# Performance work log

Hardware: AMD Instinct MI355X
Metric: run time of the kernel (lower is better)

## Reference

```python
import jax, jax.numpy as jnp
import numpy as np

NUM_SLOTS = 8
SLOT_DIM = 3
WRITE_RATE = 0.1


def _amu(x, memory, Wk, bk, Ww, bw, Wg, bg, Wo, bo):
    """Associative Memory Unit.
    x: [B, T, Din], memory: [B, N, D] -> (outputs [B, T, Dout], memory [B, N, D]).
    Per step: softmax key-addressing read, gated erase/add write at WRITE_RATE,
    output = Linear(concat(x_t, read)).
    """
    xt = jnp.swapaxes(x, 0, 1)  # [T, B, Din]

    def step(mem, x_t):
        k = x_t @ Wk + bk                                   # [B, D]
        scores = jnp.einsum('bnd,bd->bn', mem, k)           # [B, N]
        w = jax.nn.softmax(scores, axis=-1)                 # addressing weights
        read = jnp.einsum('bn,bnd->bd', w, mem)             # [B, D]
        v = x_t @ Ww + bw                                   # write vector [B, D]
        e = jax.nn.sigmoid(x_t @ Wg + bg)                   # erase gate [B, D]
        we = w[:, :, None] * e[:, None, :]                  # [B, N, D]
        mem = mem * (1.0 - WRITE_RATE * we) + WRITE_RATE * w[:, :, None] * v[:, None, :]
        out = jnp.concatenate([x_t, read], axis=-1) @ Wo + bo
        return mem, out

    mem, outs = jax.lax.scan(step, memory, xt)
    return jnp.swapaxes(outs, 0, 1), mem


def setup_inputs() -> dict:
    key = jax.random.key(0)
    ks = jax.random.split(key, 12)
    B, T, D_in, D_hid, D_out = 64, 512, 128, 512, 128
    s = 0.05
    return {
        'inp': jax.random.normal(ks[0], (B, T, D_in), jnp.float32),
        'W1k': jax.random.normal(ks[1], (D_in, SLOT_DIM), jnp.float32) * s,
        'b1k': jnp.zeros((SLOT_DIM,), jnp.float32),
        'W1w': jax.random.normal(ks[2], (D_in, SLOT_DIM), jnp.float32) * s,
        'b1w': jnp.zeros((SLOT_DIM,), jnp.float32),
        'W1g': jax.random.normal(ks[3], (D_in, SLOT_DIM), jnp.float32) * s,
        'b1g': jnp.zeros((SLOT_DIM,), jnp.float32),
        'W1o': jax.random.normal(ks[4], (D_in + SLOT_DIM, D_hid), jnp.float32) * s,
        'b1o': jnp.zeros((D_hid,), jnp.float32),
        'W2k': jax.random.normal(ks[5], (D_hid, SLOT_DIM), jnp.float32) * s,
        'b2k': jnp.zeros((SLOT_DIM,), jnp.float32),
        'W2w': jax.random.normal(ks[6], (D_hid, SLOT_DIM), jnp.float32) * s,
        'b2w': jnp.zeros((SLOT_DIM,), jnp.float32),
        'W2g': jax.random.normal(ks[7], (D_hid, SLOT_DIM), jnp.float32) * s,
        'b2g': jnp.zeros((SLOT_DIM,), jnp.float32),
        'W2o': jax.random.normal(ks[8], (D_hid + SLOT_DIM, D_out), jnp.float32) * s,
        'b2o': jnp.zeros((D_out,), jnp.float32),
    }


def reference(inp, W1k, b1k, W1w, b1w, W1g, b1g, W1o, b1o,
              W2k, b2k, W2w, b2w, W2g, b2g, W2o, b2o):
    B = inp.shape[0]
    mem0 = jnp.zeros((B, NUM_SLOTS, SLOT_DIM), inp.dtype)
    o1, mem = _amu(inp, mem0, W1k, b1k, W1w, b1w, W1g, b1g, W1o, b1o)
    o1 = jax.nn.sigmoid(o1)  # self.layers = Sequential(Sigmoid())
    o2, mem = _amu(o1, mem, W2k, b2k, W2w, b2w, W2g, b2g, W2o, b2o)
    out = jax.nn.sigmoid(o2[:, -1, :])  # last timestep, then sigmoid
    return out
```

## Files before the change

kernel.cpp:

```cpp
#include <hip/hip_runtime.h>
#include <hip/hip_bf16.h>

#define B_ 64
#define T_ 512
#define LOG2E 1.4426950408889634f
#define PHASE_STEPS 16
#define NPHASE (T_/PHASE_STEPS)

typedef __attribute__((ext_vector_type(8))) short short8;
typedef __attribute__((ext_vector_type(4))) float f32x4;

__device__ __forceinline__ float fast_exp2(float x){ return __builtin_amdgcn_exp2f(x); }
__device__ __forceinline__ float fast_rcp(float x){ return __builtin_amdgcn_rcpf(x); }
__device__ __forceinline__ float sigmoidf_(float x){ return fast_rcp(1.0f + fast_exp2(-x*LOG2E)); }
__device__ __forceinline__ unsigned short f2bf(float f){
  union{float f; unsigned u;} v; v.f = f;
  unsigned r = v.u + 0x7fffu + ((v.u>>16)&1u);
  return (unsigned short)(r>>16);
}
__device__ __forceinline__ float bf2f(unsigned short u){
  union{unsigned u; float f;} v; v.u = ((unsigned)u)<<16; return v.f;
}

template<int CTRL>
__device__ __forceinline__ float dpp_xadd(float x){
  int y = __builtin_amdgcn_update_dpp(0, __float_as_int(x), CTRL, 0xf, 0xf, true);
  return x + __int_as_float(y);
}
__device__ __forceinline__ float dpp_sum8(float x){
  x = dpp_xadd<0xB1>(x);
  x = dpp_xadd<0x4E>(x);
  x = dpp_xadd<0x141>(x);
  return x;
}

__device__ __forceinline__ void lds_barrier(){
  asm volatile("s_waitcnt lgkmcnt(0)" ::: "memory");
  __builtin_amdgcn_s_barrier();
  asm volatile("" ::: "memory");
}

__global__ __launch_bounds__(256) void k_proj1(const float* __restrict__ X,
    const float* __restrict__ Wk, const float* __restrict__ bk,
    const float* __restrict__ Ww, const float* __restrict__ bw,
    const float* __restrict__ Wg, const float* __restrict__ bg,
    float* __restrict__ P1,
    const float* __restrict__ W1o,
    const float* __restrict__ W2k, const float* __restrict__ W2w, const float* __restrict__ W2g,
    unsigned short* __restrict__ W1oTb, unsigned short* __restrict__ W2cTb)
{
  __shared__ __align__(16) float A[64*132];
  __shared__ __align__(16) float WcT[9*132];
  __shared__ float bb[9];
  int tid = threadIdx.x;
  if (blockIdx.x >= 512){
    int idx = ((int)blockIdx.x - 512)*256 + tid;
    if (idx < 65536){
      int n = idx >> 7, k = idx & 127;
      W1oTb[idx] = f2bf(W1o[k*512 + n]);
    }
    if (idx < 8192){
      int j = idx >> 9, c = idx & 511;
      float v = 0.f;
      if (j < 3) v = W2k[c*3 + j];
      else if (j < 6) v = W2w[c*3 + j - 3];
      else if (j < 9) v = W2g[c*3 + j - 6];
      W2cTb[idx] = f2bf(v);
    }
    return;
  }
  long r0 = (long)blockIdx.x * 64;
  const float4* X4 = (const float4*)(X + r0*128);
  #pragma unroll
  for (int it=0; it<8; ++it){
    int f4 = tid + it*256;
    float4 v = X4[f4];
    int f = f4*4; int row = f>>7; int k = f&127;
    *(float4*)&A[row*132+k] = v;
  }
  #pragma unroll
  for (int it=0; it<5; ++it){
    int w0 = tid + it*256;
    if (w0 < 1152){
      int k = w0/9, j = w0%9;
      float val;
      if (j<3) val = Wk[k*3+j]; else if (j<6) val = Ww[k*3+j-3]; else val = Wg[k*3+j-6];
      WcT[j*132+k] = val;
    }
  }
  if (tid < 9){
    float v; if (tid<3) v = bk[tid]; else if (tid<6) v = bw[tid-3]; else v = bg[tid-6];
    bb[tid] = v;
  }
  __syncthreads();
  for (int o = tid; o < 576; o += 256){
    int row = o/9, j = o%9;
    const f32x4* Ar = (const f32x4*)(A + row*132);
    const f32x4* Wr = (const f32x4*)(WcT + j*132);
    f32x4 acc4 = {0.f,0.f,0.f,0.f};
    #pragma unroll
    for (int k4=0;k4<32;++k4){
      f32x4 a = Ar[k4], wv = Wr[k4];
      acc4[0]=fmaf(a[0],wv[0],acc4[0]);
      acc4[1]=fmaf(a[1],wv[1],acc4[1]);
      acc4[2]=fmaf(a[2],wv[2],acc4[2]);
      acc4[3]=fmaf(a[3],wv[3],acc4[3]);
    }
    float acc = bb[j] + (acc4[0]+acc4[1]) + (acc4[2]+acc4[3]);
    if (j<3) acc *= LOG2E;
    else if (j<6) acc *= 0.1f;
    else acc = 0.1f * sigmoidf_(acc);
    long r = r0 + row;
    int b = (int)(r >> 9); int t = (int)(r & 511);
    int bh = b >> 5, bl = b & 31;
    P1[(((long)bh*512 + t)*32 + bl)*12 + j] = acc;
  }
}

template<int STORE_SM>
__device__ __forceinline__ void scan_slim(const float* __restrict__ P,
                                          float* __restrict__ Out, int bh)
{
  __shared__ __align__(16) float buf[2][PHASE_STEPS*32*12];
  int tid = threadIdx.x;
  int wv = tid >> 6, lane = tid & 63;
  const float* Pb = P + (long)bh*512*384;
  if (wv == 8){
    #pragma unroll 1
    for (int p = 0; p < NPHASE; ++p){
      const float4* s4 = (const float4*)Pb + (long)p*1536;
      float4* d4 = (float4*)buf[p&1];
      #pragma unroll
      for (int c=0;c<2;++c){
        float4 tmp[12];
        #pragma unroll
        for (int i=0;i<12;++i) tmp[i] = s4[lane + (c*12+i)*64];
        #pragma unroll
        for (int i=0;i<12;++i) d4[lane + (c*12+i)*64] = tmp[i];
      }
      lds_barrier();
    }
    return;
  }
  if (lane >= 32) return;
  int g = lane >> 3, slot = lane & 7;
  int bl = wv*4 + g;
  int batch = bh*32 + bl;
  float* So = Out + ((long)batch*8 + slot)*4;
  float m0=0.f, m1=0.f, m2=0.f;
  f32x4 pfa[4], pfb[4]; float pfc[4];
  lds_barrier();
  #pragma unroll 1
  for (int p = 0; p < NPHASE; ++p){
    const float* bp = buf[p&1] + bl*12;
    const f32x4* bp4 = (const f32x4*)bp;
    #pragma unroll
    for (int u=0;u<3;++u){
      pfa[u]=bp4[u*96]; pfb[u]=bp4[u*96+1]; pfc[u]=bp[u*384+8];
    }
    #pragma unroll
    for (int s=0;s<PHASE_STEPS;++s){
      f32x4 A0=pfa[s&3], A1=pfb[s&3]; float e2=pfc[s&3];
      if (s+3 < PHASE_STEPS){
        int i3=(s+3)&3;
        pfa[i3]=bp4[(s+3)*96]; pfb[i3]=bp4[(s+3)*96+1]; pfc[i3]=bp[(s+3)*384+8];
      }
      float sc = fmaf(m2, A0[2], fmaf(m1, A0[1], m0*A0[0]));
      float pe = fast_exp2(sc);
      float S = dpp_sum8(pe);
      float rinv = fast_rcp(S);
      float w = pe * rinv;
      if (STORE_SM){
        f32x4 sv; sv[0]=pe; sv[1]=m0; sv[2]=m1; sv[3]=m2;
        *(f32x4*)(So + (long)(p*PHASE_STEPS+s)*2048) = sv;
      } else if (p == NPHASE-1 && s == PHASE_STEPS-1){
        float r0 = dpp_sum8(pe*m0);
        float r1 = dpp_sum8(pe*m1);
        float r2 = dpp_sum8(pe*m2);
        float rsel = (slot==0) ? r0 : ((slot==1) ? r1 : r2);
        rsel *= rinv;
        if (slot < 3) Out[slot*64 + batch] = rsel;
      }
      float v0=A0[3], v1=A1[0], v2=A1[1], e0=A1[2], e1=A1[3];
      m0 = fmaf(w, fmaf(-e0, m0, v0), m0);
      m1 = fmaf(w, fmaf(-e1, m1, v1), m1);
      m2 = fmaf(w, fmaf(-e2, m2, v2), m2);
    }
    if (p < NPHASE-1) lds_barrier();
  }
}

__global__ __launch_bounds__(576) void k_scan1(const float* __restrict__ P1,
                                               float* __restrict__ SM)
{
  scan_slim<1>(P1, SM, (int)blockIdx.x);
}

__global__ __launch_bounds__(256) void k_fused(const float* __restrict__ X,
    const float* __restrict__ W1o, const float* __restrict__ b1o,
    const float* __restrict__ SM,
    const unsigned short* __restrict__ W1oTb, const unsigned short* __restrict__ W2cTb,
    const float* __restrict__ b2k, const float* __restrict__ b2w, const float* __restrict__ b2g,
    float* __restrict__ P2, float* __restrict__ O1last)
{
  __shared__ __align__(16) float rdS[192];
  __shared__ __align__(16) unsigned short o1b[64*520];
  __shared__ __align__(16) float pSum[4*16*16];
  int tid = threadIdx.x;
  int w = tid >> 6, lane = tid & 63;
  int n16 = lane & 15, g4 = lane >> 4;
  long r0 = (long)blockIdx.x * 64;
  int b = (int)(r0 >> 9); int t0 = (int)(r0 & 511);

  #pragma unroll
  for (int half=0; half<2; ++half){
    int i = (tid >> 3) + half*32;
    int slot = tid & 7;
    f32x4 v = *(const f32x4*)(SM + (((long)(t0+i)*64 + b)*8 + slot)*4);
    float S   = dpp_sum8(v[0]);
    float r0v = dpp_sum8(v[0]*v[1]);
    float r1v = dpp_sum8(v[0]*v[2]);
    float r2v = dpp_sum8(v[0]*v[3]);
    float rinv = fast_rcp(S);
    float rsel = (slot==0) ? r0v : ((slot==1) ? r1v : r2v);
    if (slot < 3) rdS[i*3+slot] = rsel*rinv;
  }

  short8 afr[4][4];
  #pragma unroll
  for (int rt=0; rt<4; ++rt){
    const float* Xrow = X + (r0 + rt*16 + n16)*128;
    #pragma unroll
    for (int q=0;q<4;++q){
      f32x4 x0 = *(const f32x4*)(Xrow + q*32 + g4*8);
      f32x4 x1 = *(const f32x4*)(Xrow + q*32 + g4*8 + 4);
      short8 a;
      a[0]=(short)f2bf(x0[0]); a[1]=(short)f2bf(x0[1]);
      a[2]=(short)f2bf(x0[2]); a[3]=(short)f2bf(x0[3]);
      a[4]=(short)f2bf(x1[0]); a[5]=(short)f2bf(x1[1]);
      a[6]=(short)f2bf(x1[2]); a[7]=(short)f2bf(x1[3]);
      afr[rt][q]=a;
    }
  }
  __syncthreads();

  #pragma unroll
  for (int tt=0; tt<8; ++tt){
    int gc = w*128 + tt*16 + n16;
    short8 bf[4];
    #pragma unroll
    for (int q=0;q<4;++q)
      bf[q] = *(const short8*)(W1oTb + gc*128 + q*32 + g4*8);
    float bias = b1o[gc];
    float wr0 = W1o[128*512+gc], wr1 = W1o[129*512+gc], wr2 = W1o[130*512+gc];
    #pragma unroll
    for (int rt=0; rt<4; ++rt){
      f32x4 acc = {0.f,0.f,0.f,0.f};
      #pragma unroll
      for (int q=0;q<4;++q)
        acc = __builtin_amdgcn_mfma_f32_16x16x32_bf16(afr[rt][q], bf[q], acc, 0,0,0);
      f32x4 ra = *(const f32x4*)(rdS + rt*48 + g4*12);
      f32x4 rb = *(const f32x4*)(rdS + rt*48 + g4*12 + 4);
      f32x4 rc = *(const f32x4*)(rdS + rt*48 + g4*12 + 8);
      float rd0[4] = { ra[0], ra[3], rb[2], rc[1] };
      float rd1[4] = { ra[1], rb[0], rb[3], rc[2] };
      float rd2[4] = { ra[2], rb[1], rc[0], rc[3] };
      #pragma unroll
      for (int reg=0; reg<4; ++reg){
        int rowloc = rt*16 + g4*4 + reg;
        float z = acc[reg] + bias + rd0[reg]*wr0 + rd1[reg]*wr1 + rd2[reg]*wr2;
        float o1 = sigmoidf_(z);
        o1b[rowloc*520 + gc] = f2bf(o1);
        if (t0 == 448 && rowloc == 63) O1last[b*512 + gc] = o1;
      }
    }
  }
  __syncthreads();

  #pragma unroll 1
  for (int rt2=0; rt2<4; ++rt2){
    f32x4 accP = {0.f,0.f,0.f,0.f};
    #pragma unroll
    for (int q2=0; q2<4; ++q2){
      int kk = w*128 + q2*32;
      short8 a2 = *(const short8*)(o1b + (rt2*16 + n16)*520 + kk + g4*8);
      short8 bb2 = *(const short8*)(W2cTb + n16*512 + kk + g4*8);
      accP = __builtin_amdgcn_mfma_f32_16x16x32_bf16(a2, bb2, accP, 0,0,0);
    }
    #pragma unroll
    for (int reg=0;reg<4;++reg){
      int rowloc = g4*4+reg;
      pSum[w*256 + rowloc*16 + n16] = accP[reg];
    }
    __syncthreads();
    if (tid < 144){
      int r = tid/9, j = tid%9;
      float s = pSum[r*16+j] + pSum[256+r*16+j] + pSum[512+r*16+j] + pSum[768+r*16+j];
      float outv;
      if (j<3){ s += b2k[j]; outv = s*LOG2E; }
      else if (j<6){ s += b2w[j-3]; outv = 0.1f*s; }
      else { s += b2g[j-6]; outv = 0.1f*sigmoidf_(s); }
      int t = t0 + rt2*16 + r;
      int bh = b >> 5, bl = b & 31;
      P2[(((long)bh*512 + t)*32 + bl)*12 + j] = outv;
    }
    __syncthreads();
  }
}

__global__ __launch_bounds__(576) void k_scan2_opart(const float* __restrict__ P2,
    float* __restrict__ R2F,
    const float* __restrict__ O1last, const float* __restrict__ W2o,
    const float* __restrict__ b2o, float* __restrict__ Opart)
{
  if (blockIdx.x < 2){
    scan_slim<0>(P2, R2F, (int)blockIdx.x);
    return;
  }
  __shared__ __align__(16) float s2[512];
  int b = blockIdx.x - 2; int tid = threadIdx.x;
  if (tid < 128)
    ((float4*)s2)[tid] = ((const float4*)(O1last + b*512))[tid];
  __syncthreads();
  if (tid < 128){
    float acc = b2o[tid];
    #pragma unroll 8
    for (int n=0;n<512;++n) acc = fmaf(s2[n], W2o[n*128+tid], acc);
    Opart[b*128+tid] = acc;
  }
}

__global__ __launch_bounds__(256) void k_final(const float* __restrict__ Opart,
    const float* __restrict__ R2F, const float* __restrict__ W2o,
    float* __restrict__ out)
{
  int idx = blockIdx.x*256 + threadIdx.x;
  if (idx < 8192){
    int b = idx >> 7; int o = idx & 127;
    float r0 = R2F[b], r1 = R2F[64+b], r2 = R2F[128+b];
    float v = Opart[idx]
            + r0*W2o[512*128+o] + r1*W2o[513*128+o] + r2*W2o[514*128+o];
    out[idx] = sigmoidf_(v);
  }
}

extern "C" void kernel_launch(void* const* d_in, const int* in_sizes, int n_in,
                              void* d_out, int out_size, void* d_ws, size_t ws_size,
                              hipStream_t stream)
{
  const float* X  = (const float*)d_in[0];
  const float* W1k= (const float*)d_in[1]; const float* b1k=(const float*)d_in[2];
  const float* W1w= (const float*)d_in[3]; const float* b1w=(const float*)d_in[4];
  const float* W1g= (const float*)d_in[5]; const float* b1g=(const float*)d_in[6];
  const float* W1o= (const float*)d_in[7]; const float* b1o=(const float*)d_in[8];
  const float* W2k= (const float*)d_in[9]; const float* b2k=(const float*)d_in[10];
  const float* W2w= (const float*)d_in[11]; const float* b2w=(const float*)d_in[12];
  const float* W2g= (const float*)d_in[13]; const float* b2g=(const float*)d_in[14];
  const float* W2o= (const float*)d_in[15]; const float* b2o=(const float*)d_in[16];

  float* ws = (float*)d_ws;
  float* P1     = ws;
  float* SM     = P1 + 393216;
  float* O1last = SM + 1048576;
  float* R2F    = O1last + 32768;
  float* Opart  = R2F + 192;
  unsigned short* W1oTb = (unsigned short*)(Opart + 8192);
  unsigned short* W2cTb = W1oTb + 65536;
  float* P2     = P1;
  float* out    = (float*)d_out;

  hipLaunchKernelGGL(k_proj1, dim3(768), dim3(256), 0, stream,
                     X, W1k,b1k, W1w,b1w, W1g,b1g, P1,
                     W1o, W2k, W2w, W2g, W1oTb, W2cTb);
  hipLaunchKernelGGL(k_scan1, dim3(2), dim3(576), 0, stream, P1, SM);
  hipLaunchKernelGGL(k_fused, dim3(512), dim3(256), 0, stream,
                     X, W1o, b1o, SM, W1oTb, W2cTb, b2k, b2w, b2g, P2, O1last);
  hipLaunchKernelGGL(k_scan2_opart, dim3(66), dim3(576), 0, stream,
                     P2, R2F, O1last, W2o, b2o, Opart);
  hipLaunchKernelGGL(k_final, dim3(32), dim3(256), 0, stream,
                     Opart, R2F, W2o, out);
}
```

Baseline: 226.0 us.

## Merge scans and fused projection into one flag-pipelined persistent kernel

Replaces the separate scan1, fused projection and scan2 launches with a single kernel. Two blocks run the first recurrent scan and publish per-chunk progress flags. Projection blocks spin on those flags before consuming softmax state, then bump counters that gate the second scan's loader warp. This lets the serial scans overlap with the bulk MFMA projection work and removes launch boundaries. The last-row output partial is also computed from LDS instead of a round trip through global memory. In exchange it relies on all producer blocks being co-resident, uses spin-waits, and writes P2 into the P1 buffer while scan1 may still be reading other timesteps of it.

```diff
diff --git a/kernel.cpp b/kernel.cpp
--- a/kernel.cpp
+++ b/kernel.cpp
@@ -6,6 +6,7 @@
 #define LOG2E 1.4426950408889634f
 #define PHASE_STEPS 16
 #define NPHASE (T_/PHASE_STEPS)
+#define AGENT_ __HIP_MEMORY_SCOPE_AGENT
 
 typedef __attribute__((ext_vector_type(8))) short short8;
 typedef __attribute__((ext_vector_type(4))) float f32x4;
@@ -40,6 +41,10 @@
   asm volatile("" ::: "memory");
 }
 
+__device__ __forceinline__ int aload(const int* p){
+  return __hip_atomic_load(p, __ATOMIC_ACQUIRE, AGENT_);
+}
+
 __global__ __launch_bounds__(256) void k_proj1(const float* __restrict__ X,
     const float* __restrict__ Wk, const float* __restrict__ bk,
     const float* __restrict__ Ww, const float* __restrict__ bw,
@@ -47,13 +52,15 @@
     float* __restrict__ P1,
     const float* __restrict__ W1o,
     const float* __restrict__ W2k, const float* __restrict__ W2w, const float* __restrict__ W2g,
-    unsigned short* __restrict__ W1oTb, unsigned short* __restrict__ W2cTb)
+    unsigned short* __restrict__ W1oTb, unsigned short* __restrict__ W2cTb,
+    int* __restrict__ flags)
 {
   __shared__ __align__(16) float A[64*132];
   __shared__ __align__(16) float WcT[9*132];
   __shared__ float bb[9];
   int tid = threadIdx.x;
   if (blockIdx.x >= 512){
+    if (blockIdx.x == 512 && tid < 18) flags[tid] = 0;
     int idx = ((int)blockIdx.x - 512)*256 + tid;
     if (idx < 65536){
       int n = idx >> 7, k = idx & 127;
@@ -117,17 +124,22 @@
   }
 }
 
-template<int STORE_SM>
-__device__ __forceinline__ void scan_slim(const float* __restrict__ P,
-                                          float* __restrict__ Out, int bh)
+template<int ROLE>
+__device__ __forceinline__ void scan_pipe(char* pool, const float* P,
+                                          float* __restrict__ Out, int bh,
+                                          int* flags)
 {
-  __shared__ __align__(16) float buf[2][PHASE_STEPS*32*12];
+  float (*buf)[PHASE_STEPS*32*12] = (float(*)[PHASE_STEPS*32*12])pool;
   int tid = threadIdx.x;
   int wv = tid >> 6, lane = tid & 63;
   const float* Pb = P + (long)bh*512*384;
   if (wv == 8){
     #pragma unroll 1
     for (int p = 0; p < NPHASE; ++p){
+      if (ROLE == 2 && (p&3)==0){
+        const int* f = flags + 2 + bh*8 + (p>>2);
+        while (aload(f) < 32) __builtin_amdgcn_s_sleep(8);
+      }
       const float4* s4 = (const float4*)Pb + (long)p*1536;
       float4* d4 = (float4*)buf[p&1];
       #pragma unroll
@@ -140,6 +152,7 @@
       }
       lds_barrier();
     }
+    if (ROLE == 1) lds_barrier();
     return;
   }
   if (lane >= 32) return;
@@ -170,7 +183,7 @@
       float S = dpp_sum8(pe);
       float rinv = fast_rcp(S);
       float w = pe * rinv;
-      if (STORE_SM){
+      if (ROLE == 1){
         f32x4 sv; sv[0]=pe; sv[1]=m0; sv[2]=m1; sv[3]=m2;
         *(f32x4*)(So + (long)(p*PHASE_STEPS+s)*2048) = sv;
       } else if (p == NPHASE-1 && s == PHASE_STEPS-1){
@@ -186,92 +199,110 @@
       m1 = fmaf(w, fmaf(-e1, m1, v1), m1);
       m2 = fmaf(w, fmaf(-e2, m2, v2), m2);
     }
+    if (ROLE == 1 && (p&3)==3)
+      asm volatile("s_waitcnt vmcnt(0)" ::: "memory");
     if (p < NPHASE-1) lds_barrier();
-  }
-}
-
-__global__ __launch_bounds__(576) void k_scan1(const float* __restrict__ P1,
-                                               float* __restrict__ SM)
-{
-  scan_slim<1>(P1, SM, (int)blockIdx.x);
-}
-
-__global__ __launch_bounds__(256) void k_fused(const float* __restrict__ X,
-    const float* __restrict__ W1o, const float* __restrict__ b1o,
-    const float* __restrict__ SM,
+    else if (ROLE == 1) lds_barrier();
+    if (ROLE == 1 && (p&3)==3 && tid==0)
+      __hip_atomic_store(&flags[bh], p+1, __ATOMIC_RELEASE, AGENT_);
+  }
+}
+
+__global__ __launch_bounds__(576) void k_pipe(
+    const float* P1, float* __restrict__ SM,
+    float* P2, float* __restrict__ R2F,
+    const float* __restrict__ X, const float* __restrict__ W1o, const float* __restrict__ b1o,
     const unsigned short* __restrict__ W1oTb, const unsigned short* __restrict__ W2cTb,
     const float* __restrict__ b2k, const float* __restrict__ b2w, const float* __restrict__ b2g,
-    float* __restrict__ P2, float* __restrict__ O1last)
+    const float* __restrict__ W2o, const float* __restrict__ b2o,
+    float* __restrict__ Opart, int* flags)
 {
-  __shared__ __align__(16) float rdS[192];
-  __shared__ __align__(16) unsigned short o1b[64*520];
-  __shared__ __align__(16) float pSum[4*16*16];
+  __shared__ __align__(16) char pool[73728];
+  int bid = blockIdx.x;
+  if (bid < 2){ scan_pipe<1>(pool, P1, SM, bid, flags); return; }
+  if (bid < 4){ scan_pipe<2>(pool, P2, R2F, bid-2, flags); return; }
+
+  float* rdS = (float*)pool;
+  unsigned short* o1b = (unsigned short*)(pool + 768);
+  float* pSum = (float*)(pool + 768 + 66560);
   int tid = threadIdx.x;
+  int c = bid - 4;
+  int b = c >> 3, q = c & 7;
+  int t0 = q*64;
+  long r0 = (long)b*512 + t0;
   int w = tid >> 6, lane = tid & 63;
   int n16 = lane & 15, g4 = lane >> 4;
-  long r0 = (long)blockIdx.x * 64;
-  int b = (int)(r0 >> 9); int t0 = (int)(r0 & 511);
-
-  #pragma unroll
-  for (int half=0; half<2; ++half){
-    int i = (tid >> 3) + half*32;
-    int slot = tid & 7;
-    f32x4 v = *(const f32x4*)(SM + (((long)(t0+i)*64 + b)*8 + slot)*4);
-    float S   = dpp_sum8(v[0]);
-    float r0v = dpp_sum8(v[0]*v[1]);
-    float r1v = dpp_sum8(v[0]*v[2]);
-    float r2v = dpp_sum8(v[0]*v[3]);
-    float rinv = fast_rcp(S);
-    float rsel = (slot==0) ? r0v : ((slot==1) ? r1v : r2v);
-    if (slot < 3) rdS[i*3+slot] = rsel*rinv;
-  }
 
   short8 afr[4][4];
-  #pragma unroll
-  for (int rt=0; rt<4; ++rt){
-    const float* Xrow = X + (r0 + rt*16 + n16)*128;
-    #pragma unroll
-    for (int q=0;q<4;++q){
-      f32x4 x0 = *(const f32x4*)(Xrow + q*32 + g4*8);
-      f32x4 x1 = *(const f32x4*)(Xrow + q*32 + g4*8 + 4);
-      short8 a;
-      a[0]=(short)f2bf(x0[0]); a[1]=(short)f2bf(x0[1]);
-      a[2]=(short)f2bf(x0[2]); a[3]=(short)f2bf(x0[3]);
-      a[4]=(short)f2bf(x1[0]); a[5]=(short)f2bf(x1[1]);
-      a[6]=(short)f2bf(x1[2]); a[7]=(short)f2bf(x1[3]);
-      afr[rt][q]=a;
+  if (tid < 256){
+    #pragma unroll
+    for (int rt=0; rt<4; ++rt){
+      const float* Xrow = X + (r0 + rt*16 + n16)*128;
+      #pragma unroll
+      for (int qq=0;qq<4;++qq){
+        f32x4 x0 = *(const f32x4*)(Xrow + qq*32 + g4*8);
+        f32x4 x1 = *(const f32x4*)(Xrow + qq*32 + g4*8 + 4);
+        short8 a;
+        a[0]=(short)f2bf(x0[0]); a[1]=(short)f2bf(x0[1]);
+        a[2]=(short)f2bf(x0[2]); a[3]=(short)f2bf(x0[3]);
+        a[4]=(short)f2bf(x1[0]); a[5]=(short)f2bf(x1[1]);
+        a[6]=(short)f2bf(x1[2]); a[7]=(short)f2bf(x1[3]);
+        afr[rt][qq]=a;
+      }
+    }
+  }
+
+  {
+    const int* sp = flags + (b>>5);
+    int need = 4*q + 4;
+    while (aload(sp) < need) __builtin_amdgcn_s_sleep(32);
+  }
+
+  if (tid < 256){
+    #pragma unroll
+    for (int half=0; half<2; ++half){
+      int i = (tid >> 3) + half*32;
+      int slot = tid & 7;
+      f32x4 v = *(const f32x4*)(SM + (((long)(t0+i)*64 + b)*8 + slot)*4);
+      float S   = dpp_sum8(v[0]);
+      float r0v = dpp_sum8(v[0]*v[1]);
+      float r1v = dpp_sum8(v[0]*v[2]);
+      float r2v = dpp_sum8(v[0]*v[3]);
+      float rinv = fast_rcp(S);
+      float rsel = (slot==0) ? r0v : ((slot==1) ? r1v : r2v);
+      if (slot < 3) rdS[i*3+slot] = rsel*rinv;
     }
   }
   __syncthreads();
 
-  #pragma unroll
-  for (int tt=0; tt<8; ++tt){
-    int gc = w*128 + tt*16 + n16;
-    short8 bf[4];
-    #pragma unroll
-    for (int q=0;q<4;++q)
-      bf[q] = *(const short8*)(W1oTb + gc*128 + q*32 + g4*8);
-    float bias = b1o[gc];
-    float wr0 = W1o[128*512+gc], wr1 = W1o[129*512+gc], wr2 = W1o[130*512+gc];
-    #pragma unroll
-    for (int rt=0; rt<4; ++rt){
-      f32x4 acc = {0.f,0.f,0.f,0.f};
-      #pragma unroll
-      for (int q=0;q<4;++q)
-        acc = __builtin_amdgcn_mfma_f32_16x16x32_bf16(afr[rt][q], bf[q], acc, 0,0,0);
-      f32x4 ra = *(const f32x4*)(rdS + rt*48 + g4*12);
-      f32x4 rb = *(const f32x4*)(rdS + rt*48 + g4*12 + 4);
-      f32x4 rc = *(const f32x4*)(rdS + rt*48 + g4*12 + 8);
-      float rd0[4] = { ra[0], ra[3], rb[2], rc[1] };
-      float rd1[4] = { ra[1], rb[0], rb[3], rc[2] };
-      float rd2[4] = { ra[2], rb[1], rc[0], rc[3] };
-      #pragma unroll
-      for (int reg=0; reg<4; ++reg){
-        int rowloc = rt*16 + g4*4 + reg;
-        float z = acc[reg] + bias + rd0[reg]*wr0 + rd1[reg]*wr1 + rd2[reg]*wr2;
-        float o1 = sigmoidf_(z);
-        o1b[rowloc*520 + gc] = f2bf(o1);
-        if (t0 == 448 && rowloc == 63) O1last[b*512 + gc] = o1;
+  if (tid < 256){
+    #pragma unroll
+    for (int tt=0; tt<8; ++tt){
+      int gc = w*128 + tt*16 + n16;
+      short8 bf[4];
+      #pragma unroll
+      for (int qq=0;qq<4;++qq)
+        bf[qq] = *(const short8*)(W1oTb + gc*128 + qq*32 + g4*8);
+      float bias = b1o[gc];
+      float wr0 = W1o[128*512+gc], wr1 = W1o[129*512+gc], wr2 = W1o[130*512+gc];
+      #pragma unroll
+      for (int rt=0; rt<4; ++rt){
+        f32x4 acc = {0.f,0.f,0.f,0.f};
+        #pragma unroll
+        for (int qq=0;qq<4;++qq)
+          acc = __builtin_amdgcn_mfma_f32_16x16x32_bf16(afr[rt][qq], bf[qq], acc, 0,0,0);
+        f32x4 ra = *(const f32x4*)(rdS + rt*48 + g4*12);
+        f32x4 rb = *(const f32x4*)(rdS + rt*48 + g4*12 + 4);
+        f32x4 rc = *(const f32x4*)(rdS + rt*48 + g4*12 + 8);
+        float rd0[4] = { ra[0], ra[3], rb[2], rc[1] };
+        float rd1[4] = { ra[1], rb[0], rb[3], rc[2] };
+        float rd2[4] = { ra[2], rb[1], rc[0], rc[3] };
+        #pragma unroll
+        for (int reg=0; reg<4; ++reg){
+          int rowloc = rt*16 + g4*4 + reg;
+          float z = acc[reg] + bias + rd0[reg]*wr0 + rd1[reg]*wr1 + rd2[reg]*wr2;
+          o1b[rowloc*520 + gc] = f2bf(sigmoidf_(z));
+        }
       }
     }
   }
@@ -279,18 +310,20 @@
 
   #pragma unroll 1
   for (int rt2=0; rt2<4; ++rt2){
-    f32x4 accP = {0.f,0.f,0.f,0.f};
-    #pragma unroll
-    for (int q2=0; q2<4; ++q2){
-      int kk = w*128 + q2*32;
-      short8 a2 = *(const short8*)(o1b + (rt2*16 + n16)*520 + kk + g4*8);
-      short8 bb2 = *(const short8*)(W2cTb + n16*512 + kk + g4*8);
-      accP = __builtin_amdgcn_mfma_f32_16x16x32_bf16(a2, bb2, accP, 0,0,0);
-    }
-    #pragma unroll
-    for (int reg=0;reg<4;++reg){
-      int rowloc = g4*4+reg;
-      pSum[w*256 + rowloc*16 + n16] = accP[reg];
+    if (tid < 256){
+      f32x4 accP = {0.f,0.f,0.f,0.f};
+      #pragma unroll
+      for (int q2=0; q2<4; ++q2){
+        int kk = w*128 + q2*32;
+        short8 a2 = *(const short8*)(o1b + (rt2*16 + n16)*520 + kk + g4*8);
+        short8 bb2 = *(const short8*)(W2cTb + n16*512 + kk + g4*8);
+        accP = __builtin_amdgcn_mfma_f32_16x16x32_bf16(a2, bb2, accP, 0,0,0);
+      }
+      #pragma unroll
+      for (int reg=0;reg<4;++reg){
+        int rowloc = g4*4+reg;
+        pSum[w*256 + rowloc*16 + n16] = accP[reg];
+      }
     }
     __syncthreads();
     if (tid < 144){
@@ -306,26 +339,15 @@
     }
     __syncthreads();
   }
-}
-
-__global__ __launch_bounds__(576) void k_scan2_opart(const float* __restrict__ P2,
-    float* __restrict__ R2F,
-    const float* __restrict__ O1last, const float* __restrict__ W2o,
-    const float* __restrict__ b2o, float* __restrict__ Opart)
-{
-  if (blockIdx.x < 2){
-    scan_slim<0>(P2, R2F, (int)blockIdx.x);
-    return;
-  }
-  __shared__ __align__(16) float s2[512];
-  int b = blockIdx.x - 2; int tid = threadIdx.x;
-  if (tid < 128)
-    ((float4*)s2)[tid] = ((const float4*)(O1last + b*512))[tid];
-  __syncthreads();
-  if (tid < 128){
+
+  if (tid == 0)
+    __hip_atomic_fetch_add(&flags[2 + (b>>5)*8 + q], 1, __ATOMIC_RELEASE, AGENT_);
+
+  if (q == 7 && tid < 128){
     float acc = b2o[tid];
     #pragma unroll 8
-    for (int n=0;n<512;++n) acc = fmaf(s2[n], W2o[n*128+tid], acc);
+    for (int n=0;n<512;++n)
+      acc = fmaf(bf2f(o1b[63*520+n]), W2o[n*128+tid], acc);
     Opart[b*128+tid] = acc;
   }
 }
@@ -361,22 +383,20 @@
   float* ws = (float*)d_ws;
   float* P1     = ws;
   float* SM     = P1 + 393216;
-  float* O1last = SM + 1048576;
-  float* R2F    = O1last + 32768;
+  float* R2F    = SM + 1048576;
   float* Opart  = R2F + 192;
   unsigned short* W1oTb = (unsigned short*)(Opart + 8192);
   unsigned short* W2cTb = W1oTb + 65536;
+  int* flags    = (int*)(W2cTb + 8192);
   float* P2     = P1;
   float* out    = (float*)d_out;
 
   hipLaunchKernelGGL(k_proj1, dim3(768), dim3(256), 0, stream,
                      X, W1k,b1k, W1w,b1w, W1g,b1g, P1,
-                     W1o, W2k, W2w, W2g, W1oTb, W2cTb);
-  hipLaunchKernelGGL(k_scan1, dim3(2), dim3(576), 0, stream, P1, SM);
-  hipLaunchKernelGGL(k_fused, dim3(512), dim3(256), 0, stream,
-                     X, W1o, b1o, SM, W1oTb, W2cTb, b2k, b2w, b2g, P2, O1last);
-  hipLaunchKernelGGL(k_scan2_opart, dim3(66), dim3(576), 0, stream,
-                     P2, R2F, O1last, W2o, b2o, Opart);
+                     W1o, W2k, W2w, W2g, W1oTb, W2cTb, flags);
+  hipLaunchKernelGGL(k_pipe, dim3(516), dim3(576), 0, stream,
+                     P1, SM, P2, R2F, X, W1o, b1o, W1oTb, W2cTb,
+                     b2k, b2w, b2g, W2o, b2o, Opart, flags);
   hipLaunchKernelGGL(k_final, dim3(32), dim3(256), 0, stream,
                      Opart, R2F, W2o, out);
 }
```

Result: slower. 464.2 us (+105.3%).
